# Kernel tuning notes

Measured on AMD Instinct MI355X. Metric: run time of the kernel, lower is better.

Reference implementation:

```python
import jax, jax.numpy as jnp
import numpy as np

B, D, NCLS = 65536, 784, 10

def sparse_layer(x, idx, w, b):
    # x: [B, D]; idx: [Dout, k] int; w: [Dout, k]; b: [Dout]
    # out[b, n] = sum_j x[b, idx[n, j]] * w[n, j] + b[n]
    g = x[:, idx]                      # [B, Dout, k] gather
    return jnp.einsum('bnk,nk->bn', g, w) + b

def setup_inputs() -> dict:
    key = jax.random.key(0)
    ks = jax.random.split(key, 12)
    def rn(k, shape, scale):
        return jax.random.normal(k, shape, dtype=jnp.float32) * scale
    return {
        'x': rn(ks[0], (B, D), 1.0),
        'idx1': jax.random.randint(ks[1], (D, 2), 0, D, dtype=jnp.int32),
        'w1': rn(ks[2], (D, 2), 0.5),
        'b1': rn(ks[3], (D,), 0.1),
        'idx2': jax.random.randint(ks[4], (D, 4), 0, D, dtype=jnp.int32),
        'w2': rn(ks[5], (D, 4), 0.4),
        'b2': rn(ks[6], (D,), 0.1),
        'idx3': jax.random.randint(ks[7], (D, 8), 0, D, dtype=jnp.int32),
        'w3': rn(ks[8], (D, 8), 0.3),
        'b3': rn(ks[9], (D,), 0.1),
        'fc_w': rn(ks[10], (NCLS, D), 0.05),
        'fc_b': rn(ks[11], (NCLS,), 0.05),
    }

def reference(x, idx1, w1, b1, idx2, w2, b2, idx3, w3, b3, fc_w, fc_b):
    h = jax.nn.gelu(sparse_layer(x, idx1, w1, b1), approximate=False)
    h = jax.nn.gelu(sparse_layer(h, idx2, w2, b2), approximate=False)
    h = jax.nn.gelu(sparse_layer(h, idx3, w3, b3), approximate=False)
    logits = h @ fc_w.T + fc_b          # [B, 10]
    return jax.nn.softmax(logits, axis=-1)
```

## Files before the change

### kernel.cpp

```cpp
#include <hip/hip_runtime.h>

#define D_     784
#define ROWS   8
#define NCLS   10
#define BLOCK  768
#define NB     (65536 / ROWS)
#define PL     (D_ * 4)
#define TAIL   (D_ - BLOCK)

__device__ __forceinline__ float gelu_f(float x) {
    float x2    = x * x;
    float inner = fmaf(0.044715f * x, x2, x);
    float e     = exp2f(2.3022082f * inner);
    float r     = __builtin_amdgcn_rcpf(e + 1.0f);
    return fmaf(-x, r, x);
}

__device__ __forceinline__ float4 gelu4(const float4& a) {
    return make_float4(gelu_f(a.x), gelu_f(a.y), gelu_f(a.z), gelu_f(a.w));
}

__device__ __forceinline__ void fma4(float4& a, const float4& h4, float wk) {
    a.x = fmaf(h4.x, wk, a.x);
    a.y = fmaf(h4.y, wk, a.y);
    a.z = fmaf(h4.z, wk, a.z);
    a.w = fmaf(h4.w, wk, a.w);
}

template <int K>
__device__ __forceinline__ void loadIdxW(const int* __restrict__ idx,
                                         const float* __restrict__ w,
                                         int n, int* jc, float* wc) {
    if constexpr (K == 2) {
        int2   j = *(const int2*)(idx + n * 2);
        float2 v = *(const float2*)(w + n * 2);
        jc[0] = j.x; jc[1] = j.y; wc[0] = v.x; wc[1] = v.y;
    } else if constexpr (K == 4) {
        int4   j = *(const int4*)(idx + n * 4);
        float4 v = *(const float4*)(w + n * 4);
        jc[0] = j.x; jc[1] = j.y; jc[2] = j.z; jc[3] = j.w;
        wc[0] = v.x; wc[1] = v.y; wc[2] = v.z; wc[3] = v.w;
    } else {
        int4   ja = *(const int4*)(idx + n * 8);
        int4   jb = *(const int4*)(idx + n * 8 + 4);
        float4 va = *(const float4*)(w + n * 8);
        float4 vb = *(const float4*)(w + n * 8 + 4);
        jc[0] = ja.x; jc[1] = ja.y; jc[2] = ja.z; jc[3] = ja.w;
        jc[4] = jb.x; jc[5] = jb.y; jc[6] = jb.z; jc[7] = jb.w;
        wc[0] = va.x; wc[1] = va.y; wc[2] = va.z; wc[3] = va.w;
        wc[4] = vb.x; wc[5] = vb.y; wc[6] = vb.z; wc[7] = vb.w;
    }
}

template <int K>
__device__ __forceinline__ void layer_one(const float* __restrict__ src,
                                          float* __restrict__ dst,
                                          const int* __restrict__ idx,
                                          const float* __restrict__ w,
                                          const float* __restrict__ bias,
                                          int n) {
    int   jc[K];
    float wc[K];
    loadIdxW<K>(idx, w, n, jc, wc);
    float  bc = bias[n];
    float4 lo = make_float4(bc, bc, bc, bc);
    float4 hi = lo;
#pragma unroll
    for (int k = 0; k < K; ++k) {
        const float* g = src + jc[k] * 4;
        float4 gl = *(const float4*)g;
        float4 gh = *(const float4*)(g + PL);
        fma4(lo, gl, wc[k]);
        fma4(hi, gh, wc[k]);
    }
    *(float4*)(dst + n * 4)      = gelu4(lo);
    *(float4*)(dst + n * 4 + PL) = gelu4(hi);
}

__global__ __launch_bounds__(BLOCK)
void circnn_kernel(const float* __restrict__ x,
                   const int* __restrict__ idx1, const float* __restrict__ w1, const float* __restrict__ b1,
                   const int* __restrict__ idx2, const float* __restrict__ w2, const float* __restrict__ b2,
                   const int* __restrict__ idx3, const float* __restrict__ w3, const float* __restrict__ b3,
                   const float* __restrict__ fcw, const float* __restrict__ fcb,
                   float* __restrict__ out) {
    __shared__ __align__(16) float bufA[D_ * ROWS];
    __shared__ __align__(16) float bufB[D_ * ROWS];
    __shared__ float logits[ROWS * NCLS];

    const int tid  = threadIdx.x;
    const int row0 = blockIdx.x * ROWS;

    const float* xb = x + (size_t)row0 * D_;
    {
        int n = tid;
        float4 lo, hi;
        lo.x = xb[0 * D_ + n]; lo.y = xb[1 * D_ + n];
        lo.z = xb[2 * D_ + n]; lo.w = xb[3 * D_ + n];
        hi.x = xb[4 * D_ + n]; hi.y = xb[5 * D_ + n];
        hi.z = xb[6 * D_ + n]; hi.w = xb[7 * D_ + n];
        *(float4*)(bufA + n * 4)      = lo;
        *(float4*)(bufA + n * 4 + PL) = hi;
    }
    if (tid < TAIL) {
        int n = BLOCK + tid;
        float4 lo, hi;
        lo.x = xb[0 * D_ + n]; lo.y = xb[1 * D_ + n];
        lo.z = xb[2 * D_ + n]; lo.w = xb[3 * D_ + n];
        hi.x = xb[4 * D_ + n]; hi.y = xb[5 * D_ + n];
        hi.z = xb[6 * D_ + n]; hi.w = xb[7 * D_ + n];
        *(float4*)(bufA + n * 4)      = lo;
        *(float4*)(bufA + n * 4 + PL) = hi;
    }
    __syncthreads();

    layer_one<2>(bufA, bufB, idx1, w1, b1, tid);
    if (tid < TAIL) layer_one<2>(bufA, bufB, idx1, w1, b1, BLOCK + tid);
    __syncthreads();

    layer_one<4>(bufB, bufA, idx2, w2, b2, tid);
    if (tid < TAIL) layer_one<4>(bufB, bufA, idx2, w2, b2, BLOCK + tid);
    __syncthreads();

    layer_one<8>(bufA, bufB, idx3, w3, b3, tid);
    if (tid < TAIL) layer_one<8>(bufA, bufB, idx3, w3, b3, BLOCK + tid);
    __syncthreads();

    float4* part4 = (float4*)bufA;
    if (tid < 128) {
        const int jj = tid >> 1;
        const int qq = tid & 1;
        float4 facc[NCLS];
#pragma unroll
        for (int c = 0; c < NCLS; ++c) facc[c] = make_float4(0.f, 0.f, 0.f, 0.f);
#pragma unroll 1
        for (int i = 0; i < 13; ++i) {
            int n = jj + 64 * i;
            if (n < D_) {
                float4 hv = *(const float4*)(bufB + qq * PL + n * 4);
#pragma unroll
                for (int c = 0; c < NCLS; ++c)
                    fma4(facc[c], hv, fcw[c * D_ + n]);
            }
        }
#pragma unroll
        for (int c = 0; c < NCLS; ++c)
            part4[(jj * 2 + qq) * NCLS + c] = facc[c];
    }
    __syncthreads();

    if (tid < ROWS * NCLS) {
        int r = tid / NCLS, c = tid - r * NCLS;
        int qq = r >> 2, comp = r & 3;
        const float* pf = (const float*)part4;
        float s = fcb[c];
#pragma unroll 4
        for (int jj = 0; jj < 64; ++jj)
            s += pf[((jj * 2 + qq) * NCLS + c) * 4 + comp];
        logits[tid] = s;
    }
    __syncthreads();

    if (tid < ROWS * NCLS) {
        int r = tid / NCLS;
        const float* lg = logits + r * NCLS;
        float m = lg[0];
#pragma unroll
        for (int c = 1; c < NCLS; ++c) m = fmaxf(m, lg[c]);
        float s = 0.f;
#pragma unroll
        for (int c = 0; c < NCLS; ++c) s += __expf(lg[c] - m);
        out[(size_t)row0 * NCLS + tid] = __expf(logits[tid] - m) / s;
    }
}

extern "C" void kernel_launch(void* const* d_in, const int* in_sizes, int n_in,
                              void* d_out, int out_size, void* d_ws, size_t ws_size,
                              hipStream_t stream) {
    const float* x    = (const float*)d_in[0];
    const int*   idx1 = (const int*)d_in[1];
    const float* w1   = (const float*)d_in[2];
    const float* b1   = (const float*)d_in[3];
    const int*   idx2 = (const int*)d_in[4];
    const float* w2   = (const float*)d_in[5];
    const float* b2   = (const float*)d_in[6];
    const int*   idx3 = (const int*)d_in[7];
    const float* w3   = (const float*)d_in[8];
    const float* b3   = (const float*)d_in[9];
    const float* fcw  = (const float*)d_in[10];
    const float* fcb  = (const float*)d_in[11];
    float* out = (float*)d_out;

    circnn_kernel<<<dim3(NB), dim3(BLOCK), 0, stream>>>(
        x, idx1, w1, b1, idx2, w2, b2, idx3, w3, b3, fcw, fcb, out);
}
```

Before: 428.2 us.

## Make kernel persistent with register-cached sparse weights and prefetched next-row tile

Launches a fixed grid of 512 blocks that each loop over 16 row-groups. The per-thread index, weight and bias values for the three sparse layers are loaded once into registers, and the tail is remapped to the last 16 threads. The next group's input rows are loaded into registers during the current group's compute and stored into shared memory after layer 3. This removes repeated idx/weight loads and block launch overhead and tries to hide global load latency, at the cost of more registers and a separate shared buffer for the FC partials.

```diff
diff --git a/kernel.cpp b/kernel.cpp
--- a/kernel.cpp
+++ b/kernel.cpp
@@ -4,9 +4,11 @@
 #define ROWS   8
 #define NCLS   10
 #define BLOCK  768
+#define CPB    512
 #define NB     (65536 / ROWS)
+#define NITER  (NB / CPB)
 #define PL     (D_ * 4)
-#define TAIL   (D_ - BLOCK)
+#define TAILN  16
 
 __device__ __forceinline__ float gelu_f(float x) {
     float x2    = x * x;
@@ -53,6 +55,23 @@
 }
 
 template <int K>
+__device__ __forceinline__ void layer_reg(const float* __restrict__ src,
+                                          float* __restrict__ dst,
+                                          const int (&jc)[K], const float (&wc)[K],
+                                          float bc, int n) {
+    float4 lo = make_float4(bc, bc, bc, bc);
+    float4 hi = lo;
+#pragma unroll
+    for (int k = 0; k < K; ++k) {
+        const float* g = src + jc[k] * 4;
+        fma4(lo, *(const float4*)g, wc[k]);
+        fma4(hi, *(const float4*)(g + PL), wc[k]);
+    }
+    *(float4*)(dst + n * 4)      = gelu4(lo);
+    *(float4*)(dst + n * 4 + PL) = gelu4(hi);
+}
+
+template <int K>
 __device__ __forceinline__ void layer_one(const float* __restrict__ src,
                                           float* __restrict__ dst,
                                           const int* __restrict__ idx,
@@ -62,22 +81,10 @@
     int   jc[K];
     float wc[K];
     loadIdxW<K>(idx, w, n, jc, wc);
-    float  bc = bias[n];
-    float4 lo = make_float4(bc, bc, bc, bc);
-    float4 hi = lo;
-#pragma unroll
-    for (int k = 0; k < K; ++k) {
-        const float* g = src + jc[k] * 4;
-        float4 gl = *(const float4*)g;
-        float4 gh = *(const float4*)(g + PL);
-        fma4(lo, gl, wc[k]);
-        fma4(hi, gh, wc[k]);
-    }
-    *(float4*)(dst + n * 4)      = gelu4(lo);
-    *(float4*)(dst + n * 4 + PL) = gelu4(hi);
-}
-
-__global__ __launch_bounds__(BLOCK)
+    layer_reg<K>(src, dst, jc, wc, bias[n], n);
+}
+
+__global__ __launch_bounds__(BLOCK, 6)
 void circnn_kernel(const float* __restrict__ x,
                    const int* __restrict__ idx1, const float* __restrict__ w1, const float* __restrict__ b1,
                    const int* __restrict__ idx2, const float* __restrict__ w2, const float* __restrict__ b2,
@@ -86,91 +93,113 @@
                    float* __restrict__ out) {
     __shared__ __align__(16) float bufA[D_ * ROWS];
     __shared__ __align__(16) float bufB[D_ * ROWS];
+    __shared__ __align__(16) float partC[128 * NCLS * 4];
     __shared__ float logits[ROWS * NCLS];
 
-    const int tid  = threadIdx.x;
-    const int row0 = blockIdx.x * ROWS;
-
-    const float* xb = x + (size_t)row0 * D_;
+    const int tid = threadIdx.x;
+
+    int   j1[2], j2[4], j3[8];
+    float v1[2], v2[4], v3[8];
+    loadIdxW<2>(idx1, w1, tid, j1, v1);
+    loadIdxW<4>(idx2, w2, tid, j2, v2);
+    loadIdxW<8>(idx3, w3, tid, j3, v3);
+    const float bb1 = b1[tid], bb2 = b2[tid], bb3 = b3[tid];
+
+    const bool isTail = (tid >= BLOCK - TAILN);
+    const int  ntail  = tid + TAILN;
+
+    const int xtN = 768 + (tid >> 3);
+    const int xtR = tid & 7;
+
     {
-        int n = tid;
-        float4 lo, hi;
-        lo.x = xb[0 * D_ + n]; lo.y = xb[1 * D_ + n];
-        lo.z = xb[2 * D_ + n]; lo.w = xb[3 * D_ + n];
-        hi.x = xb[4 * D_ + n]; hi.y = xb[5 * D_ + n];
-        hi.z = xb[6 * D_ + n]; hi.w = xb[7 * D_ + n];
-        *(float4*)(bufA + n * 4)      = lo;
-        *(float4*)(bufA + n * 4 + PL) = hi;
-    }
-    if (tid < TAIL) {
-        int n = BLOCK + tid;
-        float4 lo, hi;
-        lo.x = xb[0 * D_ + n]; lo.y = xb[1 * D_ + n];
-        lo.z = xb[2 * D_ + n]; lo.w = xb[3 * D_ + n];
-        hi.x = xb[4 * D_ + n]; hi.y = xb[5 * D_ + n];
-        hi.z = xb[6 * D_ + n]; hi.w = xb[7 * D_ + n];
-        *(float4*)(bufA + n * 4)      = lo;
-        *(float4*)(bufA + n * 4 + PL) = hi;
+        const float* xb = x + (size_t)blockIdx.x * ROWS * D_;
+        float r0 = xb[0 * D_ + tid], r1 = xb[1 * D_ + tid];
+        float r2 = xb[2 * D_ + tid], r3 = xb[3 * D_ + tid];
+        float r4 = xb[4 * D_ + tid], r5 = xb[5 * D_ + tid];
+        float r6 = xb[6 * D_ + tid], r7 = xb[7 * D_ + tid];
+        *(float4*)(bufA + tid * 4)      = make_float4(r0, r1, r2, r3);
+        *(float4*)(bufA + tid * 4 + PL) = make_float4(r4, r5, r6, r7);
+        if (tid < 128)
+            bufA[xtN * 4 + (xtR & 3) + (xtR >> 2) * PL] = xb[xtR * D_ + xtN];
     }
     __syncthreads();
 
-    layer_one<2>(bufA, bufB, idx1, w1, b1, tid);
-    if (tid < TAIL) layer_one<2>(bufA, bufB, idx1, w1, b1, BLOCK + tid);
-    __syncthreads();
-
-    layer_one<4>(bufB, bufA, idx2, w2, b2, tid);
-    if (tid < TAIL) layer_one<4>(bufB, bufA, idx2, w2, b2, BLOCK + tid);
-    __syncthreads();
-
-    layer_one<8>(bufA, bufB, idx3, w3, b3, tid);
-    if (tid < TAIL) layer_one<8>(bufA, bufB, idx3, w3, b3, BLOCK + tid);
-    __syncthreads();
-
-    float4* part4 = (float4*)bufA;
-    if (tid < 128) {
-        const int jj = tid >> 1;
-        const int qq = tid & 1;
-        float4 facc[NCLS];
-#pragma unroll
-        for (int c = 0; c < NCLS; ++c) facc[c] = make_float4(0.f, 0.f, 0.f, 0.f);
 #pragma unroll 1
-        for (int i = 0; i < 13; ++i) {
-            int n = jj + 64 * i;
-            if (n < D_) {
-                float4 hv = *(const float4*)(bufB + qq * PL + n * 4);
-#pragma unroll
-                for (int c = 0; c < NCLS; ++c)
-                    fma4(facc[c], hv, fcw[c * D_ + n]);
+    for (int it = 0; it < NITER; ++it) {
+        const size_t grp  = (size_t)it * CPB + blockIdx.x;
+        float nx0, nx1, nx2, nx3, nx4, nx5, nx6, nx7, nxt;
+        if (it + 1 < NITER) {
+            const float* xb = x + ((size_t)(it + 1) * CPB + blockIdx.x) * ROWS * D_;
+            nx0 = xb[0 * D_ + tid]; nx1 = xb[1 * D_ + tid];
+            nx2 = xb[2 * D_ + tid]; nx3 = xb[3 * D_ + tid];
+            nx4 = xb[4 * D_ + tid]; nx5 = xb[5 * D_ + tid];
+            nx6 = xb[6 * D_ + tid]; nx7 = xb[7 * D_ + tid];
+            nxt = (tid < 128) ? xb[xtR * D_ + xtN] : 0.f;
+        }
+
+        layer_reg<2>(bufA, bufB, j1, v1, bb1, tid);
+        if (isTail) layer_one<2>(bufA, bufB, idx1, w1, b1, ntail);
+        __syncthreads();
+
+        layer_reg<4>(bufB, bufA, j2, v2, bb2, tid);
+        if (isTail) layer_one<4>(bufB, bufA, idx2, w2, b2, ntail);
+        __syncthreads();
+
+        layer_reg<8>(bufA, bufB, j3, v3, bb3, tid);
+        if (isTail) layer_one<8>(bufA, bufB, idx3, w3, b3, ntail);
+        __syncthreads();
+        if (it + 1 < NITER) {
+            *(float4*)(bufA + tid * 4)      = make_float4(nx0, nx1, nx2, nx3);
+            *(float4*)(bufA + tid * 4 + PL) = make_float4(nx4, nx5, nx6, nx7);
+            if (tid < 128)
+                bufA[xtN * 4 + (xtR & 3) + (xtR >> 2) * PL] = nxt;
+        }
+
+        float4* part4 = (float4*)partC;
+        if (tid < 128) {
+            const int jj = tid >> 1;
+            const int qq = tid & 1;
+            float4 facc[NCLS];
+#pragma unroll
+            for (int c = 0; c < NCLS; ++c) facc[c] = make_float4(0.f, 0.f, 0.f, 0.f);
+#pragma unroll 1
+            for (int i = 0; i < 13; ++i) {
+                int n = jj + 64 * i;
+                if (n < D_) {
+                    float4 hv = *(const float4*)(bufB + qq * PL + n * 4);
+#pragma unroll
+                    for (int c = 0; c < NCLS; ++c)
+                        fma4(facc[c], hv, fcw[c * D_ + n]);
+                }
             }
-        }
-#pragma unroll
-        for (int c = 0; c < NCLS; ++c)
-            part4[(jj * 2 + qq) * NCLS + c] = facc[c];
-    }
-    __syncthreads();
-
-    if (tid < ROWS * NCLS) {
-        int r = tid / NCLS, c = tid - r * NCLS;
-        int qq = r >> 2, comp = r & 3;
-        const float* pf = (const float*)part4;
-        float s = fcb[c];
+#pragma unroll
+            for (int c = 0; c < NCLS; ++c)
+                part4[(jj * 2 + qq) * NCLS + c] = facc[c];
+        }
+        __syncthreads();
+
+        if (tid < ROWS * NCLS) {
+            int r = tid / NCLS, c = tid - r * NCLS;
+            int qq = r >> 2, comp = r & 3;
+            float s = fcb[c];
 #pragma unroll 4
-        for (int jj = 0; jj < 64; ++jj)
-            s += pf[((jj * 2 + qq) * NCLS + c) * 4 + comp];
-        logits[tid] = s;
-    }
-    __syncthreads();
-
-    if (tid < ROWS * NCLS) {
-        int r = tid / NCLS;
-        const float* lg = logits + r * NCLS;
-        float m = lg[0];
-#pragma unroll
-        for (int c = 1; c < NCLS; ++c) m = fmaxf(m, lg[c]);
-        float s = 0.f;
-#pragma unroll
-        for (int c = 0; c < NCLS; ++c) s += __expf(lg[c] - m);
-        out[(size_t)row0 * NCLS + tid] = __expf(logits[tid] - m) / s;
+            for (int jj = 0; jj < 64; ++jj)
+                s += partC[((jj * 2 + qq) * NCLS + c) * 4 + comp];
+            logits[tid] = s;
+        }
+        __syncthreads();
+
+        if (tid < ROWS * NCLS) {
+            int r = tid / NCLS;
+            const float* lg = logits + r * NCLS;
+            float m = lg[0];
+#pragma unroll
+            for (int c = 1; c < NCLS; ++c) m = fmaxf(m, lg[c]);
+            float s = 0.f;
+#pragma unroll
+            for (int c = 0; c < NCLS; ++c) s += __expf(lg[c] - m);
+            out[grp * ROWS * NCLS + tid] = __expf(logits[tid] - m) / s;
+        }
     }
 }
 
@@ -191,6 +220,6 @@
     const float* fcb  = (const float*)d_in[11];
     float* out = (float*)d_out;
 
-    circnn_kernel<<<dim3(NB), dim3(BLOCK), 0, stream>>>(
+    circnn_kernel<<<dim3(CPB), dim3(BLOCK), 0, stream>>>(
         x, idx1, w1, b1, idx2, w2, b2, idx3, w3, b3, fcw, fcb, out);
 }
```

Measured after the change: 989.3 us. +131.0%, slower.
